# Kernel optimization log

Hardware: AMD Instinct MI355X
Metric: run time of the kernel (lower is better)

## Reference

```python
import jax, jax.numpy as jnp
import numpy as np

B, D_IN, D_OUT, W = 16, 1024, 1024, 2048


def setup_inputs() -> dict:
    key = jax.random.key(0)
    kq, kk, kv, kwq, kwk, kwv = jax.random.split(key, 6)
    scale = 1.0 / np.sqrt(D_IN).astype(np.float32)
    return {
        "Q": jax.random.normal(kq, (B, D_IN, W), jnp.float32),
        "K": jax.random.normal(kk, (B, D_IN, W), jnp.float32),
        "V": jax.random.normal(kv, (B, D_IN, W), jnp.float32),
        "WQ": jax.random.normal(kwq, (D_OUT, D_IN), jnp.float32) * scale,
        "WK": jax.random.normal(kwk, (D_OUT, D_IN), jnp.float32) * scale,
        "WV": jax.random.normal(kwv, (D_OUT, D_IN), jnp.float32) * scale,
    }


def reference(Q, K, V, WQ, WK, WV):
    # Projections: M @ x with x laid out (B, d_in, seq) -> (B, d_out, seq)
    Qd = jnp.einsum('oi,bis->bos', WQ, Q)
    Kd = jnp.einsum('oi,bis->bos', WK, K)
    Vd = jnp.einsum('oi,bis->bos', WV, V)
    d_out = Qd.shape[1]
    seq = Qd.shape[2]
    # corr_mat[b, s(query), t(key)] = Q_d^T @ K_d / sqrt(d_out)
    scores = jnp.einsum('bos,bot->bst', Qd, Kd) / jnp.asarray(d_out, jnp.float32) ** 0.5
    # causal_factor = tril(-inf, diag=-1): -inf where query s > key t
    idx = jnp.arange(seq)
    mask = jnp.where(idx[:, None] > idx[None, :], -jnp.inf, 0.0).astype(scores.dtype)
    scores = scores + mask
    # NOTE: original softmaxes over dim 1 = the QUERY axis
    p = jax.nn.softmax(scores, axis=1)
    # V_d @ softmaxed -> (B, d_out, seq) indexed by key positions
    return jnp.einsum('bos,bst->bot', Vd, p)
```

## Files before the change

kernel.cpp:

```cpp
#include <hip/hip_runtime.h>
#include <cstdio>
#include <math.h>

typedef unsigned short u16;
typedef float f32x4 __attribute__((ext_vector_type(4)));
typedef __bf16 bf16x8 __attribute__((ext_vector_type(8)));
typedef u16 u16x4 __attribute__((ext_vector_type(4)));
typedef u16 u16x8 __attribute__((ext_vector_type(8)));

__device__ __forceinline__ u16 f2bf(float x) {
  unsigned u = __float_as_uint(x);
  u = (u + 0x7FFFu + ((u >> 16) & 1u)) >> 16;
  return (u16)u;
}
__device__ __forceinline__ float bf2f(u16 x) {
  return __uint_as_float(((unsigned)x) << 16);
}

__device__ __forceinline__ f32x4 mfma_bf16(bf16x8 a, bf16x8 b, f32x4 c) {
  return __builtin_amdgcn_mfma_f32_16x16x32_bf16(a, b, c, 0, 0, 0);
}

__device__ __forceinline__ void gload_lds16(const void* g, void* l) {
  __builtin_amdgcn_global_load_lds(
      (const __attribute__((address_space(1))) void*)g,
      (__attribute__((address_space(3))) void*)l, 16, 0, 0);
}

template <bool BF16OUT, bool XSWZ, bool TRI, bool KLIMIT, bool SWAPXY>
__global__ __launch_bounds__(512, 2) void gemm_bt(
    const u16* __restrict__ A, const u16* __restrict__ B, void* __restrict__ Cv,
    int K, int lda, int ldb, int ldc,
    long long sAz, long long sBz, long long sCz, float scale)
{
  int bx, by;
  if (TRI) {
    const int j = blockIdx.x;
    int r = (int)(0.5f * (sqrtf(4.f * j + 1.f) - 1.f));
    while (r * (r + 1) > j) --r;
    while ((r + 1) * (r + 2) <= j) ++r;
    by = r;
    bx = j - r * (r + 1);
  } else if (SWAPXY) {
    bx = blockIdx.y; by = blockIdx.x;
  } else if (XSWZ) {
    const int gx = gridDim.x;
    const int nwg = gx * gridDim.y;
    const int f0 = blockIdx.x + gx * blockIdx.y;
    const int f = (f0 & 7) * (nwg >> 3) + (f0 >> 3);
    bx = f & (gx - 1);
    by = f / gx;
  } else {
    bx = blockIdx.x; by = blockIdx.y;
  }

  const int n0 = bx * 128;
  const int m0 = by * 256;
  const int z = blockIdx.z;
  A += (long long)z * sAz;
  B += (long long)z * sBz;

  const int tid = threadIdx.x;
  const int wave = tid >> 6, lane = tid & 63;
  const int wr = wave >> 1, wc = wave & 1;

  __shared__ u16 lds[3][24576];

  f32x4 acc[4][4] = {};

  int kEnd = K;
  if (KLIMIT) { int ke = n0 + 128; kEnd = ke < K ? ke : K; }
  const int nt = kEnd >> 6;

  const int sOff = ((lane & 7) ^ ((lane >> 3) & 7)) * 8;
  const u16* gAs = A + (long long)(m0 + (lane >> 3)) * lda + sOff;
  const u16* gBs = B + (long long)(n0 + (lane >> 3)) * ldb + sOff;

  const int frow = lane & 15, g = lane >> 4, swz = frow & 7;
  const int aoff0 = (wr * 64 + frow) * 64 + ((g    ) ^ swz) * 8;
  const int aoff1 = (wr * 64 + frow) * 64 + ((4 + g) ^ swz) * 8;
  const int boff0 = 16384 + (wc * 64 + frow) * 64 + ((g    ) ^ swz) * 8;
  const int boff1 = 16384 + (wc * 64 + frow) * 64 + ((4 + g) ^ swz) * 8;

#define STAGE_A(T, BUF)                                                        \
  {                                                                            \
    const long long kc = (long long)(T) * 64;                                  \
    _Pragma("unroll")                                                          \
    for (int j = 0; j < 4; ++j) {                                              \
      const int c = j * 8 + wave;                                              \
      gload_lds16(gAs + (long long)(c * 8) * lda + kc, &lds[BUF][c * 512]);    \
    }                                                                          \
  }
#define STAGE_B(T, BUF)                                                        \
  {                                                                            \
    const long long kc = (long long)(T) * 64;                                  \
    _Pragma("unroll")                                                          \
    for (int j = 0; j < 2; ++j) {                                              \
      const int c = j * 8 + wave;                                              \
      gload_lds16(gBs + (long long)(c * 8) * ldb + kc,                         \
                  &lds[BUF][16384 + c * 512]);                                 \
    }                                                                          \
  }

  STAGE_A(0, 0) STAGE_B(0, 0)
  if (nt > 1) {
    STAGE_A(1, 1) STAGE_B(1, 1)
    asm volatile("s_waitcnt vmcnt(6)" ::: "memory");
  } else {
    asm volatile("s_waitcnt vmcnt(0)" ::: "memory");
  }
  __builtin_amdgcn_s_barrier();

  int cur = 0, nxt = 2;
  for (int t = 0; t < nt; ++t) {
    const u16* bb = &lds[cur][0];
    const bool pf = (t + 2 < nt);
    bf16x8 A0[4], A1[4], B0k0[2], B0k1[2], B1k0[2], B1k1[2];

#pragma unroll
    for (int m = 0; m < 4; ++m) {
      A0[m] = *(const bf16x8*)(bb + aoff0 + m * 1024);
      A1[m] = *(const bf16x8*)(bb + aoff1 + m * 1024);
    }
#pragma unroll
    for (int n = 0; n < 2; ++n) {
      B0k0[n] = *(const bf16x8*)(bb + boff0 + n * 1024);
      B0k1[n] = *(const bf16x8*)(bb + boff1 + n * 1024);
    }
    if (pf) STAGE_A(t + 2, nxt)
    __builtin_amdgcn_s_barrier();
    __builtin_amdgcn_s_setprio(1);
#pragma unroll
    for (int m = 0; m < 4; ++m)
#pragma unroll
      for (int n = 0; n < 2; ++n)
        acc[m][n] = mfma_bf16(A0[m], B0k0[n], acc[m][n]);
#pragma unroll
    for (int m = 0; m < 4; ++m)
#pragma unroll
      for (int n = 0; n < 2; ++n)
        acc[m][n] = mfma_bf16(A1[m], B0k1[n], acc[m][n]);
    __builtin_amdgcn_s_setprio(0);
    __builtin_amdgcn_s_barrier();

#pragma unroll
    for (int n = 0; n < 2; ++n) {
      B1k0[n] = *(const bf16x8*)(bb + boff0 + (2 + n) * 1024);
      B1k1[n] = *(const bf16x8*)(bb + boff1 + (2 + n) * 1024);
    }
    if (pf) STAGE_B(t + 2, nxt)
    __builtin_amdgcn_s_barrier();
    __builtin_amdgcn_s_setprio(1);
#pragma unroll
    for (int m = 0; m < 4; ++m)
#pragma unroll
      for (int n = 0; n < 2; ++n)
        acc[m][n + 2] = mfma_bf16(A0[m], B1k0[n], acc[m][n + 2]);
#pragma unroll
    for (int m = 0; m < 4; ++m)
#pragma unroll
      for (int n = 0; n < 2; ++n)
        acc[m][n + 2] = mfma_bf16(A1[m], B1k1[n], acc[m][n + 2]);
    __builtin_amdgcn_s_setprio(0);
    if (pf) asm volatile("s_waitcnt vmcnt(6)" ::: "memory");
    else    asm volatile("s_waitcnt vmcnt(0)" ::: "memory");
    __builtin_amdgcn_s_barrier();
    cur = (cur == 2) ? 0 : cur + 1;
    nxt = (nxt == 2) ? 0 : nxt + 1;
  }
#undef STAGE_A
#undef STAGE_B

  const int crow0 = m0 + wr * 64 + (lane >> 4) * 4;
  const int ccol0 = n0 + wc * 64 + (lane & 15);
  if (BF16OUT) {
    u16* C = (u16*)Cv + (long long)z * sCz;
#pragma unroll
    for (int m = 0; m < 4; ++m)
#pragma unroll
      for (int n = 0; n < 4; ++n)
#pragma unroll
        for (int r = 0; r < 4; ++r)
          C[(long long)(crow0 + m * 16 + r) * ldc + ccol0 + n * 16] = f2bf(acc[m][n][r] * scale);
  } else {
    float* C = (float*)Cv + (long long)z * sCz;
#pragma unroll
    for (int m = 0; m < 4; ++m)
#pragma unroll
      for (int n = 0; n < 4; ++n)
#pragma unroll
        for (int r = 0; r < 4; ++r)
          C[(long long)(crow0 + m * 16 + r) * ldc + ccol0 + n * 16] = acc[m][n][r] * scale;
  }
}

__global__ __launch_bounds__(256) void conv_transpose(const float* __restrict__ src, u16* __restrict__ dst)
{
  const int b = blockIdx.z;
  const float* s = src + (long long)b * 1024 * 2048;
  u16* d = dst + (long long)b * 2048 * 1024;
  const int s0 = blockIdx.x * 64, i0 = blockIdx.y * 64;
  const int tx = threadIdx.x, ty = threadIdx.y;
  __shared__ float tile[64][65];
#pragma unroll
  for (int r = 0; r < 16; ++r)
    tile[r * 4 + ty][tx] = s[(long long)(i0 + r * 4 + ty) * 2048 + s0 + tx];
  __syncthreads();
#pragma unroll
  for (int r = 0; r < 16; ++r)
    d[(long long)(s0 + r * 4 + ty) * 1024 + i0 + tx] = f2bf(tile[tx][r * 4 + ty]);
}

__global__ __launch_bounds__(256) void conv_weights(
    const float* __restrict__ a, const float* __restrict__ b, const float* __restrict__ c,
    u16* __restrict__ oa, u16* __restrict__ ob, u16* __restrict__ oc)
{
  const int which = blockIdx.y;
  const float* s = which == 0 ? a : which == 1 ? b : c;
  u16* d = which == 0 ? oa : which == 1 ? ob : oc;
  const int idx = (blockIdx.x * 256 + threadIdx.x) * 4;
  f32x4 v = *(const f32x4*)(s + idx);
  u16x4 o;
#pragma unroll
  for (int j = 0; j < 4; ++j) o[j] = f2bf(v[j]);
  *(u16x4*)(d + idx) = o;
}

__global__ __launch_bounds__(256) void col_softmax(const u16* __restrict__ S, u16* __restrict__ P)
{
  const int t = blockIdx.x;
  const long long rowOff = ((long long)blockIdx.y * 2048 + t) * 2048;
  const u16* row = S + rowOff;
  u16* prow = P + rowOff;
  const int tid = threadIdx.x;
  const int i0 = tid * 8;

  u16x8 a = *(const u16x8*)(row + i0);
  float v[8];
#pragma unroll
  for (int j = 0; j < 8; ++j)
    v[j] = (i0 + j <= t) ? bf2f(a[j]) : -1e30f;

  float m = v[0];
#pragma unroll
  for (int j = 1; j < 8; ++j) m = fmaxf(m, v[j]);
#pragma unroll
  for (int off = 32; off; off >>= 1) m = fmaxf(m, __shfl_xor(m, off));
  __shared__ float red[4];
  __shared__ float red2[4];
  if ((tid & 63) == 0) red[tid >> 6] = m;
  __syncthreads();
  m = fmaxf(fmaxf(red[0], red[1]), fmaxf(red[2], red[3]));

  float e[8]; float ssum = 0.f;
#pragma unroll
  for (int j = 0; j < 8; ++j) { e[j] = __expf(v[j] - m); ssum += e[j]; }
#pragma unroll
  for (int off = 32; off; off >>= 1) ssum += __shfl_xor(ssum, off);
  if ((tid & 63) == 0) red2[tid >> 6] = ssum;
  __syncthreads();
  ssum = red2[0] + red2[1] + red2[2] + red2[3];
  const float inv = 1.0f / ssum;
  u16x8 o;
#pragma unroll
  for (int j = 0; j < 8; ++j) o[j] = f2bf(e[j] * inv);
  *(u16x8*)(prow + i0) = o;
}

extern "C" void kernel_launch(void* const* d_in, const int* in_sizes, int n_in,
                              void* d_out, int out_size, void* d_ws, size_t ws_size,
                              hipStream_t stream)
{
  const float* Q  = (const float*)d_in[0];
  const float* K  = (const float*)d_in[1];
  const float* V  = (const float*)d_in[2];
  const float* WQ = (const float*)d_in[3];
  const float* WK = (const float*)d_in[4];
  const float* WV = (const float*)d_in[5];
  float* out = (float*)d_out;

  const size_t MB = 1ull << 20;
  char* w = (char*)d_ws;
  if (ws_size < 262 * MB) {
    fprintf(stderr, "kernel_launch: workspace too small (%zu B, need >= %zu B)\n",
            ws_size, (size_t)(262 * MB));
    return;
  }

  u16* wq    = (u16*)(w + 0 * MB);
  u16* wk    = (u16*)(w + 2 * MB);
  u16* wv    = (u16*)(w + 4 * MB);
  u16* qdt   = (u16*)(w + 6 * MB);
  u16* kdt   = (u16*)(w + 70 * MB);
  u16* vd    = (u16*)(w + 134 * MB);
  u16* trans = (u16*)(w + 198 * MB);
  u16* S     = (u16*)(w + 198 * MB);

  long long freeMB = (long long)(ws_size / MB) - 198;
  int chunk = (int)(freeMB / 16);
  if (chunk > 8) chunk = 8;
  u16* P = (u16*)(w + (198 + (size_t)chunk * 8) * MB);

  conv_weights<<<dim3(1024, 3), 256, 0, stream>>>(WQ, WK, WV, wq, wk, wv);

  conv_transpose<<<dim3(32, 16, 16), dim3(64, 4), 0, stream>>>(Q, trans);
  gemm_bt<true, true, false, false, false><<<dim3(8, 128, 1), 512, 0, stream>>>(
      trans, wq, qdt, 1024, 1024, 1024, 1024, 0, 0, 0, 1.0f);
  conv_transpose<<<dim3(32, 16, 16), dim3(64, 4), 0, stream>>>(K, trans);
  gemm_bt<true, true, false, false, false><<<dim3(8, 128, 1), 512, 0, stream>>>(
      trans, wk, kdt, 1024, 1024, 1024, 1024, 0, 0, 0, 1.0f);
  conv_transpose<<<dim3(32, 16, 16), dim3(64, 4), 0, stream>>>(V, trans);
  gemm_bt<true, true, false, false, false><<<dim3(16, 4, 16), 512, 0, stream>>>(
      wv, trans, vd, 1024, 1024, 1024, 2048,
      0, (long long)2048 * 1024, (long long)1024 * 2048, 1.0f);

  for (int b0 = 0; b0 < 16; b0 += chunk) {
    const int nb = (16 - b0) < chunk ? (16 - b0) : chunk;
    gemm_bt<true, false, true, false, false><<<dim3(72, 1, nb), 512, 0, stream>>>(
        kdt + (long long)b0 * 2048 * 1024, qdt + (long long)b0 * 2048 * 1024, S,
        1024, 1024, 1024, 2048,
        (long long)2048 * 1024, (long long)2048 * 1024, (long long)2048 * 2048, 0.03125f);
    col_softmax<<<dim3(2048, nb), 256, 0, stream>>>(S, P);
    gemm_bt<false, false, false, true, true><<<dim3(4, 16, nb), 512, 0, stream>>>(
        vd + (long long)b0 * 1024 * 2048, P, out + (long long)b0 * 1024 * 2048,
        2048, 2048, 2048, 2048,
        (long long)1024 * 2048, (long long)2048 * 2048, (long long)1024 * 2048, 1.0f);
  }
}
```

Before: 682.0 us.

## Enlarge GEMM tiles to 256x256 with 4-stage K=32 pipeline

Changes the shared bf16 GEMM kernel from 256x128 output tiles with K-step 64 and triple buffering to 256x256 tiles with K-step 32 and four LDS buffers (prefetch depth 3). The wave layout becomes 2x4, with each wave owning 128x64 of the output. The triangular tile mapping and all grid sizes are updated to match. The goal is higher arithmetic intensity per LDS byte and deeper latency hiding. In exchange each wave holds twice the accumulators, which raises register pressure and may lower occupancy, and the grids have fewer blocks.

Result: no change. 683.1 us (+0.2%).

```diff
diff --git a/kernel.cpp b/kernel.cpp
--- a/kernel.cpp
+++ b/kernel.cpp
@@ -36,11 +36,11 @@
   int bx, by;
   if (TRI) {
     const int j = blockIdx.x;
-    int r = (int)(0.5f * (sqrtf(4.f * j + 1.f) - 1.f));
-    while (r * (r + 1) > j) --r;
-    while ((r + 1) * (r + 2) <= j) ++r;
+    int r = (int)((sqrtf(8.f * j + 1.f) - 1.f) * 0.5f);
+    while (r * (r + 1) / 2 > j) --r;
+    while ((r + 1) * (r + 2) / 2 <= j) ++r;
     by = r;
-    bx = j - r * (r + 1);
+    bx = j - r * (r + 1) / 2;
   } else if (SWAPXY) {
     bx = blockIdx.y; by = blockIdx.x;
   } else if (XSWZ) {
@@ -54,7 +54,7 @@
     bx = blockIdx.x; by = blockIdx.y;
   }
 
-  const int n0 = bx * 128;
+  const int n0 = bx * 256;
   const int m0 = by * 256;
   const int z = blockIdx.z;
   A += (long long)z * sAz;
@@ -62,121 +62,96 @@
 
   const int tid = threadIdx.x;
   const int wave = tid >> 6, lane = tid & 63;
-  const int wr = wave >> 1, wc = wave & 1;
-
-  __shared__ u16 lds[3][24576];
-
-  f32x4 acc[4][4] = {};
+  const int wr = wave >> 2, wc = wave & 3;
+
+  __shared__ u16 lds[4][16384];
+
+  f32x4 acc[8][4] = {};
 
   int kEnd = K;
-  if (KLIMIT) { int ke = n0 + 128; kEnd = ke < K ? ke : K; }
-  const int nt = kEnd >> 6;
-
-  const int sOff = ((lane & 7) ^ ((lane >> 3) & 7)) * 8;
-  const u16* gAs = A + (long long)(m0 + (lane >> 3)) * lda + sOff;
-  const u16* gBs = B + (long long)(n0 + (lane >> 3)) * ldb + sOff;
-
-  const int frow = lane & 15, g = lane >> 4, swz = frow & 7;
-  const int aoff0 = (wr * 64 + frow) * 64 + ((g    ) ^ swz) * 8;
-  const int aoff1 = (wr * 64 + frow) * 64 + ((4 + g) ^ swz) * 8;
-  const int boff0 = 16384 + (wc * 64 + frow) * 64 + ((g    ) ^ swz) * 8;
-  const int boff1 = 16384 + (wc * 64 + frow) * 64 + ((4 + g) ^ swz) * 8;
+  if (KLIMIT) { int ke = n0 + 256; kEnd = ke < K ? ke : K; }
+  const int nt = kEnd >> 5;
+
+  const int sOff = ((lane & 3) ^ ((lane >> 3) & 3)) * 8;
+  const u16* gAs = A + (long long)(m0 + wave * 16 + (lane >> 2)) * lda + sOff;
+  const u16* gBs = B + (long long)(n0 + wave * 16 + (lane >> 2)) * ldb + sOff;
+
+  const int frow = lane & 15, g = lane >> 4;
+  const int ps = g ^ ((frow >> 1) & 3);
+  const int aBase = (wr * 128 + frow) * 32 + ps * 8;
+  const int bBase = 8192 + (wc * 64 + frow) * 32 + ps * 8;
 
 #define STAGE_A(T, BUF)                                                        \
   {                                                                            \
-    const long long kc = (long long)(T) * 64;                                  \
+    const long long kc = (long long)(T) * 32;                                  \
     _Pragma("unroll")                                                          \
-    for (int j = 0; j < 4; ++j) {                                              \
-      const int c = j * 8 + wave;                                              \
-      gload_lds16(gAs + (long long)(c * 8) * lda + kc, &lds[BUF][c * 512]);    \
-    }                                                                          \
+    for (int c = 0; c < 2; ++c)                                                \
+      gload_lds16(gAs + (long long)(c * 128) * lda + kc,                       \
+                  &lds[BUF][c * 4096 + wave * 512]);                           \
   }
 #define STAGE_B(T, BUF)                                                        \
   {                                                                            \
-    const long long kc = (long long)(T) * 64;                                  \
+    const long long kc = (long long)(T) * 32;                                  \
     _Pragma("unroll")                                                          \
-    for (int j = 0; j < 2; ++j) {                                              \
-      const int c = j * 8 + wave;                                              \
-      gload_lds16(gBs + (long long)(c * 8) * ldb + kc,                         \
-                  &lds[BUF][16384 + c * 512]);                                 \
-    }                                                                          \
+    for (int c = 0; c < 2; ++c)                                                \
+      gload_lds16(gBs + (long long)(c * 128) * ldb + kc,                       \
+                  &lds[BUF][8192 + c * 4096 + wave * 512]);                    \
   }
 
   STAGE_A(0, 0) STAGE_B(0, 0)
-  if (nt > 1) {
-    STAGE_A(1, 1) STAGE_B(1, 1)
-    asm volatile("s_waitcnt vmcnt(6)" ::: "memory");
-  } else {
-    asm volatile("s_waitcnt vmcnt(0)" ::: "memory");
-  }
+  STAGE_A(1, 1) STAGE_B(1, 1)
+  STAGE_A(2, 2) STAGE_B(2, 2)
+  asm volatile("s_waitcnt vmcnt(8)" ::: "memory");
   __builtin_amdgcn_s_barrier();
 
-  int cur = 0, nxt = 2;
+  int cur = 0, nxt = 3;
   for (int t = 0; t < nt; ++t) {
     const u16* bb = &lds[cur][0];
-    const bool pf = (t + 2 < nt);
-    bf16x8 A0[4], A1[4], B0k0[2], B0k1[2], B1k0[2], B1k1[2];
-
-#pragma unroll
-    for (int m = 0; m < 4; ++m) {
-      A0[m] = *(const bf16x8*)(bb + aoff0 + m * 1024);
-      A1[m] = *(const bf16x8*)(bb + aoff1 + m * 1024);
-    }
-#pragma unroll
-    for (int n = 0; n < 2; ++n) {
-      B0k0[n] = *(const bf16x8*)(bb + boff0 + n * 1024);
-      B0k1[n] = *(const bf16x8*)(bb + boff1 + n * 1024);
-    }
-    if (pf) STAGE_A(t + 2, nxt)
+    const int rem = nt - 1 - t;
+    bf16x8 af[4], bf[4];
+
+#pragma unroll
+    for (int m = 0; m < 4; ++m) af[m] = *(const bf16x8*)(bb + aBase + m * 512);
+#pragma unroll
+    for (int n = 0; n < 4; ++n) bf[n] = *(const bf16x8*)(bb + bBase + n * 512);
+    if (rem >= 3) STAGE_A(t + 3, nxt)
     __builtin_amdgcn_s_barrier();
     __builtin_amdgcn_s_setprio(1);
 #pragma unroll
     for (int m = 0; m < 4; ++m)
 #pragma unroll
-      for (int n = 0; n < 2; ++n)
-        acc[m][n] = mfma_bf16(A0[m], B0k0[n], acc[m][n]);
-#pragma unroll
-    for (int m = 0; m < 4; ++m)
-#pragma unroll
-      for (int n = 0; n < 2; ++n)
-        acc[m][n] = mfma_bf16(A1[m], B0k1[n], acc[m][n]);
+      for (int n = 0; n < 4; ++n)
+        acc[m][n] = mfma_bf16(af[m], bf[n], acc[m][n]);
     __builtin_amdgcn_s_setprio(0);
     __builtin_amdgcn_s_barrier();
 
 #pragma unroll
-    for (int n = 0; n < 2; ++n) {
-      B1k0[n] = *(const bf16x8*)(bb + boff0 + (2 + n) * 1024);
-      B1k1[n] = *(const bf16x8*)(bb + boff1 + (2 + n) * 1024);
-    }
-    if (pf) STAGE_B(t + 2, nxt)
+    for (int m = 0; m < 4; ++m) af[m] = *(const bf16x8*)(bb + aBase + (4 + m) * 512);
+    if (rem >= 3) STAGE_B(t + 3, nxt)
     __builtin_amdgcn_s_barrier();
     __builtin_amdgcn_s_setprio(1);
 #pragma unroll
     for (int m = 0; m < 4; ++m)
 #pragma unroll
-      for (int n = 0; n < 2; ++n)
-        acc[m][n + 2] = mfma_bf16(A0[m], B1k0[n], acc[m][n + 2]);
-#pragma unroll
-    for (int m = 0; m < 4; ++m)
-#pragma unroll
-      for (int n = 0; n < 2; ++n)
-        acc[m][n + 2] = mfma_bf16(A1[m], B1k1[n], acc[m][n + 2]);
+      for (int n = 0; n < 4; ++n)
+        acc[4 + m][n] = mfma_bf16(af[m], bf[n], acc[4 + m][n]);
     __builtin_amdgcn_s_setprio(0);
-    if (pf) asm volatile("s_waitcnt vmcnt(6)" ::: "memory");
-    else    asm volatile("s_waitcnt vmcnt(0)" ::: "memory");
+    if (rem >= 3)      asm volatile("s_waitcnt vmcnt(8)" ::: "memory");
+    else if (rem == 2) asm volatile("s_waitcnt vmcnt(4)" ::: "memory");
+    else               asm volatile("s_waitcnt vmcnt(0)" ::: "memory");
     __builtin_amdgcn_s_barrier();
-    cur = (cur == 2) ? 0 : cur + 1;
-    nxt = (nxt == 2) ? 0 : nxt + 1;
+    cur = (cur + 1) & 3;
+    nxt = (nxt + 1) & 3;
   }
 #undef STAGE_A
 #undef STAGE_B
 
-  const int crow0 = m0 + wr * 64 + (lane >> 4) * 4;
+  const int crow0 = m0 + wr * 128 + (lane >> 4) * 4;
   const int ccol0 = n0 + wc * 64 + (lane & 15);
   if (BF16OUT) {
     u16* C = (u16*)Cv + (long long)z * sCz;
 #pragma unroll
-    for (int m = 0; m < 4; ++m)
+    for (int m = 0; m < 8; ++m)
 #pragma unroll
       for (int n = 0; n < 4; ++n)
 #pragma unroll
@@ -185,7 +160,7 @@
   } else {
     float* C = (float*)Cv + (long long)z * sCz;
 #pragma unroll
-    for (int m = 0; m < 4; ++m)
+    for (int m = 0; m < 8; ++m)
 #pragma unroll
       for (int n = 0; n < 4; ++n)
 #pragma unroll
@@ -304,24 +279,24 @@
   conv_weights<<<dim3(1024, 3), 256, 0, stream>>>(WQ, WK, WV, wq, wk, wv);
 
   conv_transpose<<<dim3(32, 16, 16), dim3(64, 4), 0, stream>>>(Q, trans);
-  gemm_bt<true, true, false, false, false><<<dim3(8, 128, 1), 512, 0, stream>>>(
+  gemm_bt<true, true, false, false, false><<<dim3(4, 128, 1), 512, 0, stream>>>(
       trans, wq, qdt, 1024, 1024, 1024, 1024, 0, 0, 0, 1.0f);
   conv_transpose<<<dim3(32, 16, 16), dim3(64, 4), 0, stream>>>(K, trans);
-  gemm_bt<true, true, false, false, false><<<dim3(8, 128, 1), 512, 0, stream>>>(
+  gemm_bt<true, true, false, false, false><<<dim3(4, 128, 1), 512, 0, stream>>>(
       trans, wk, kdt, 1024, 1024, 1024, 1024, 0, 0, 0, 1.0f);
   conv_transpose<<<dim3(32, 16, 16), dim3(64, 4), 0, stream>>>(V, trans);
-  gemm_bt<true, true, false, false, false><<<dim3(16, 4, 16), 512, 0, stream>>>(
+  gemm_bt<true, false, false, false, false><<<dim3(8, 4, 16), 512, 0, stream>>>(
       wv, trans, vd, 1024, 1024, 1024, 2048,
       0, (long long)2048 * 1024, (long long)1024 * 2048, 1.0f);
 
   for (int b0 = 0; b0 < 16; b0 += chunk) {
     const int nb = (16 - b0) < chunk ? (16 - b0) : chunk;
-    gemm_bt<true, false, true, false, false><<<dim3(72, 1, nb), 512, 0, stream>>>(
+    gemm_bt<true, false, true, false, false><<<dim3(36, 1, nb), 512, 0, stream>>>(
         kdt + (long long)b0 * 2048 * 1024, qdt + (long long)b0 * 2048 * 1024, S,
         1024, 1024, 1024, 2048,
         (long long)2048 * 1024, (long long)2048 * 1024, (long long)2048 * 2048, 0.03125f);
     col_softmax<<<dim3(2048, nb), 256, 0, stream>>>(S, P);
-    gemm_bt<false, false, false, true, true><<<dim3(4, 16, nb), 512, 0, stream>>>(
+    gemm_bt<false, false, false, true, true><<<dim3(4, 8, nb), 512, 0, stream>>>(
         vd + (long long)b0 * 1024 * 2048, P, out + (long long)b0 * 1024 * 2048,
         2048, 2048, 2048, 2048,
         (long long)1024 * 2048, (long long)2048 * 2048, (long long)1024 * 2048, 1.0f);
```
